# Optimization experiments

Hardware: AMD Instinct MI355X
Metric: run time of the kernel (lower is better)

Reference implementation:

```python
import jax, jax.numpy as jnp
import numpy as np

B, T, C = 8, 512, 2048          # batch streams, qlen, hidden_size
H, Z = 32, 64                   # num_heads, head_size; A = H*Z = attention_hidden_size
A = H * Z
TMX, TDX = 32, 64               # TIME_MIX_EXTRA_DIM, TIME_DECAY_EXTRA_DIM
EPS = 1e-5 * 8.0**2             # ln_x eps = 1e-5 * head_size_divisor**2


def setup_inputs() -> dict:
    key = jax.random.key(0)
    ks = jax.random.split(key, 24)
    def rn(i, shape, scale=1.0):
        return jax.random.normal(ks[i], shape, jnp.float32) * scale
    inv_c = 1.0 / np.sqrt(C)
    return {
        "hidden_states": rn(0, (B * T, C)),
        "positions": jnp.zeros((B * T,), jnp.int32),
        "input_kv_state": jnp.zeros((B, H, Z, Z), jnp.float32),
        "input_shift_state": rn(1, (B, C)),
        "time_maa_x": rn(2, (1, 1, C), 0.1),
        "time_maa_w": rn(3, (1, 1, C), 0.1),
        "time_maa_k": rn(4, (1, 1, C), 0.1),
        "time_maa_v": rn(5, (1, 1, C), 0.1),
        "time_maa_r": rn(6, (1, 1, C), 0.1),
        "time_maa_g": rn(7, (1, 1, C), 0.1),
        "time_maa_w1": rn(8, (C, TMX * 5), inv_c),
        "time_maa_w2": rn(9, (5, TMX, C), 1.0 / np.sqrt(TMX)),
        "time_decay": rn(10, (1, 1, A), 0.5),
        "time_decay_w1": rn(11, (C, TDX), inv_c),
        "time_decay_w2": rn(12, (TDX, A), 0.01),
        "time_faaaa": rn(13, (H, Z), 0.1),
        "W_r": rn(14, (C, A), inv_c),
        "W_k": rn(15, (C, A), inv_c),
        "W_v": rn(16, (C, A), inv_c),
        "W_g": rn(17, (C, A), inv_c),
        "W_o": rn(18, (A, C), inv_c),
        "ln_w": 1.0 + rn(19, (C,), 0.1),
        "ln_b": rn(20, (C,), 0.1),
    }


def _rwkv6_forward(hidden_states, positions, input_kv_state, input_shift_state,
                   time_maa_x, time_maa_w, time_maa_k, time_maa_v, time_maa_r,
                   time_maa_g, time_maa_w1, time_maa_w2, time_decay,
                   time_decay_w1, time_decay_w2, time_faaaa,
                   W_r, W_k, W_v, W_g, W_o, ln_w, ln_b):
    x = hidden_states.reshape(B, T, C)
    pos0_is_zero = positions.reshape(B, T)[:, 0] == 0
    reset = jnp.where(pos0_is_zero, -100.0, 0.0)  # [B]
    # kill shift state for fresh sequences (matches * exp(-100))
    shift = input_shift_state * jnp.exp(reset)[:, None]  # [B, C]

    # token-shift mixing (shift state broadcast over T, as in source)
    xx = shift[:, None, :] - x  # [B, T, C]
    xxx = x + xx * time_maa_x
    mix = jnp.tanh(xxx @ time_maa_w1).reshape(B, T, 5, TMX)
    mix = jnp.einsum('btfe,fec->fbtc', mix, time_maa_w2)  # [5, B, T, C]
    mw, mk, mv, mr, mg = mix

    td_in = x + xx * (time_maa_w + mw)
    kx = x + xx * (time_maa_k + mk)
    vx = x + xx * (time_maa_v + mv)
    rx = x + xx * (time_maa_r + mr)
    gx = x + xx * (time_maa_g + mg)

    r = rx @ W_r
    k = kx @ W_k
    v = vx @ W_v
    g = jax.nn.silu(gx @ W_g)  # [B, T, A]

    w = time_decay + jnp.tanh(td_in @ time_decay_w1) @ time_decay_w2
    w = -jnp.exp(w.astype(jnp.float32))  # log-decay, [B, T, A]

    # split heads -> [T, B, H, Z] for scan
    def to_tbhz(a):
        return a.reshape(B, T, H, Z).transpose(1, 0, 2, 3)
    r_s, k_s, v_s, w_s = to_tbhz(r), to_tbhz(k), to_tbhz(v), to_tbhz(w)
    # zero out carried state at t=0 for fresh sequences
    w_s = w_s.at[0].add(reset[:, None, None])

    u = time_faaaa  # [H, Z]

    def step(S, rkvw):
        # S: [B, H, K, V] (key-dim x value-dim state)
        r_t, k_t, v_t, w_t = rkvw  # each [B, H, Z]
        kv = k_t[..., :, None] * v_t[..., None, :]  # [B, H, K, V]
        o = jnp.einsum('bhk,bhkv->bhv', r_t, S + u[None, :, :, None] * kv)
        S = jnp.exp(w_t)[..., None] * S + kv
        return S, o

    S_out, o = jax.lax.scan(step, input_kv_state, (r_s, k_s, v_s, w_s))
    xo = o.transpose(1, 0, 2, 3).reshape(B * T, C)  # [B*T, C]

    # GroupNorm over heads (num_groups = H)
    xg = xo.reshape(B * T, H, Z)
    mu = xg.mean(-1, keepdims=True)
    var = xg.var(-1, keepdims=True)
    xn = ((xg - mu) * jax.lax.rsqrt(var + EPS)).reshape(B * T, C) * ln_w + ln_b

    out = (xn.reshape(B, T, C) * g) @ W_o  # [B, T, C]
    return out.reshape(B * T, C)


def reference(hidden_states, positions, input_kv_state, input_shift_state,
              time_maa_x, time_maa_w, time_maa_k, time_maa_v, time_maa_r,
              time_maa_g, time_maa_w1, time_maa_w2, time_decay,
              time_decay_w1, time_decay_w2, time_faaaa,
              W_r, W_k, W_v, W_g, W_o, ln_w, ln_b):
    return _rwkv6_forward(hidden_states, positions, input_kv_state,
                          input_shift_state, time_maa_x, time_maa_w,
                          time_maa_k, time_maa_v, time_maa_r, time_maa_g,
                          time_maa_w1, time_maa_w2, time_decay, time_decay_w1,
                          time_decay_w2, time_faaaa, W_r, W_k, W_v, W_g, W_o,
                          ln_w, ln_b)
```

## Files before the change

### kernel.cpp

```cpp
#include <hip/hip_runtime.h>
#include <cmath>

#define NB 8
#define NT 512
#define NC 2048
#define NH 32
#define NZ 64
static constexpr float GN_EPS = 1e-5f * 64.0f;

typedef _Float16 f16;
typedef __attribute__((ext_vector_type(8))) _Float16 f16x8;
typedef __attribute__((ext_vector_type(4))) _Float16 f16x4;
typedef __attribute__((ext_vector_type(4))) float f4;

static __device__ __forceinline__ void gload16(const void* gp, void* lp) {
  __builtin_amdgcn_global_load_lds(
      (const __attribute__((address_space(1))) void*)gp,
      (__attribute__((address_space(3))) void*)lp, 16, 0, 0);
}

__global__ void k_transpose_cast(const float* __restrict__ in, f16* __restrict__ out,
                                 int R, int Cc) {
  __shared__ float tile[32][33];
  int c0 = blockIdx.x * 32, r0 = blockIdx.y * 32;
  int tx = threadIdx.x, ty = threadIdx.y;
#pragma unroll
  for (int i = 0; i < 4; ++i)
    tile[ty + i * 8][tx] = in[(size_t)(r0 + ty + i * 8) * Cc + c0 + tx];
  __syncthreads();
#pragma unroll
  for (int i = 0; i < 4; ++i)
    out[(size_t)(c0 + ty + i * 8) * R + r0 + tx] = (f16)tile[tx][ty + i * 8];
}

__global__ void k_transpose_split(const float* __restrict__ in, f16* __restrict__ ohi,
                                  f16* __restrict__ olo, int R, int Cc) {
  __shared__ float tile[32][33];
  int c0 = blockIdx.x * 32, r0 = blockIdx.y * 32;
  int tx = threadIdx.x, ty = threadIdx.y;
#pragma unroll
  for (int i = 0; i < 4; ++i)
    tile[ty + i * 8][tx] = in[(size_t)(r0 + ty + i * 8) * Cc + c0 + tx];
  __syncthreads();
#pragma unroll
  for (int i = 0; i < 4; ++i) {
    float v = tile[tx][ty + i * 8];
    f16 h = (f16)v;
    size_t o = (size_t)(c0 + ty + i * 8) * R + r0 + tx;
    ohi[o] = h;
    olo[o] = (f16)(v - (float)h);
  }
}

__global__ void k_xxx(const float* __restrict__ hs, const float* __restrict__ shift_st,
                      const int* __restrict__ positions, const float* __restrict__ maa_x,
                      float* __restrict__ xxx) {
  int i = blockIdx.x * blockDim.x + threadIdx.x;
  int idx = i * 4;
  int c = idx & (NC - 1);
  int t = idx >> 11;
  int b = t >> 9;
  float er = (positions[b * NT] == 0) ? expf(-100.0f) : 1.0f;
  const float4 x = *(const float4*)(hs + idx);
  const float4 sh = *(const float4*)(shift_st + b * NC + c);
  const float4 mx = *(const float4*)(maa_x + c);
  float4 o;
  o.x = x.x + (sh.x * er - x.x) * mx.x;
  o.y = x.y + (sh.y * er - x.y) * mx.y;
  o.z = x.z + (sh.z * er - x.z) * mx.z;
  o.w = x.w + (sh.w * er - x.w) * mx.w;
  *(float4*)(xxx + idx) = o;
}

static __device__ __forceinline__ void split4(const float4 v, int base, f16x8& hi, f16x8& lo) {
  float x[4] = {v.x, v.y, v.z, v.w};
#pragma unroll
  for (int j = 0; j < 4; ++j) {
    f16 h = (f16)x[j];
    hi[base + j] = h;
    lo[base + j] = (f16)(x[j] - (float)h);
  }
}

__global__ __launch_bounds__(64) void k_mix1_split(const float* __restrict__ A,
                                                   const f16* __restrict__ Bhi,
                                                   const f16* __restrict__ Blo,
                                                   float* __restrict__ out) {
  int m0 = blockIdx.x * 16, n0 = blockIdx.y * 16;
  int lane = threadIdx.x, lr = lane & 15, kq = lane >> 4;
  f4 acc = {0.f, 0.f, 0.f, 0.f};
  const float* ap = A + (size_t)(m0 + lr) * 2048 + kq * 8;
  const f16* bh0 = Bhi + (size_t)(n0 + lr) * 2048 + kq * 8;
  const f16* bl0 = Blo + (size_t)(n0 + lr) * 2048 + kq * 8;
  for (int k0 = 0; k0 < 2048; k0 += 32) {
    f16x8 ah, al;
    split4(*(const float4*)(ap + k0), 0, ah, al);
    split4(*(const float4*)(ap + k0 + 4), 4, ah, al);
    f16x8 bh = *(const f16x8*)(bh0 + k0);
    f16x8 bl = *(const f16x8*)(bl0 + k0);
    acc = __builtin_amdgcn_mfma_f32_16x16x32_f16(ah, bh, acc, 0, 0, 0);
    acc = __builtin_amdgcn_mfma_f32_16x16x32_f16(ah, bl, acc, 0, 0, 0);
    acc = __builtin_amdgcn_mfma_f32_16x16x32_f16(al, bh, acc, 0, 0, 0);
  }
#pragma unroll
  for (int r = 0; r < 4; ++r)
    out[(size_t)(m0 + kq * 4 + r) * 160 + n0 + lr] = tanhf(acc[r]);
}

__global__ __launch_bounds__(64) void k_tmp5_split(const float* __restrict__ mixb,
    const f16* __restrict__ Bhi, const f16* __restrict__ Blo,
    const float* __restrict__ hs, const float* __restrict__ shift_st,
    const int* __restrict__ positions,
    const float* __restrict__ maa_w, const float* __restrict__ maa_k,
    const float* __restrict__ maa_v, const float* __restrict__ maa_r,
    const float* __restrict__ maa_g,
    float* __restrict__ tdin, f16* __restrict__ kx, f16* __restrict__ vx,
    f16* __restrict__ rx, f16* __restrict__ gx) {
  int m0 = blockIdx.x * 16, n0 = blockIdx.y * 16;
  int lane = threadIdx.x, lr = lane & 15, kq = lane >> 4;
  f4 acc[5];
#pragma unroll
  for (int f = 0; f < 5; ++f) acc[f] = (f4){0.f, 0.f, 0.f, 0.f};
  const float* ap = mixb + (size_t)(m0 + lr) * 160 + kq * 8;
#pragma unroll
  for (int f = 0; f < 5; ++f) {
    f16x8 ah, al;
    split4(*(const float4*)(ap + f * 32), 0, ah, al);
    split4(*(const float4*)(ap + f * 32 + 4), 4, ah, al);
    size_t bi = ((size_t)f * 2048 + n0 + lr) * 32 + kq * 8;
    f16x8 bh = *(const f16x8*)(Bhi + bi);
    f16x8 bl = *(const f16x8*)(Blo + bi);
    acc[f] = __builtin_amdgcn_mfma_f32_16x16x32_f16(ah, bh, acc[f], 0, 0, 0);
    acc[f] = __builtin_amdgcn_mfma_f32_16x16x32_f16(ah, bl, acc[f], 0, 0, 0);
    acc[f] = __builtin_amdgcn_mfma_f32_16x16x32_f16(al, bh, acc[f], 0, 0, 0);
  }
  int c = n0 + lr;
  float mw = maa_w[c], mk = maa_k[c], mv = maa_v[c], mr = maa_r[c], mg = maa_g[c];
#pragma unroll
  for (int r = 0; r < 4; ++r) {
    int t = m0 + kq * 4 + r;
    int b = t >> 9;
    float er = (positions[b * NT] == 0) ? expf(-100.0f) : 1.0f;
    float x = hs[(size_t)t * NC + c];
    float xxv = shift_st[b * NC + c] * er - x;
    size_t oi = (size_t)t * NC + c;
    tdin[oi] = x + xxv * (mw + acc[0][r]);
    kx[oi] = (f16)(x + xxv * (mk + acc[1][r]));
    vx[oi] = (f16)(x + xxv * (mv + acc[2][r]));
    rx[oi] = (f16)(x + xxv * (mr + acc[3][r]));
    gx[oi] = (f16)(x + xxv * (mg + acc[4][r]));
  }
}

__global__ __launch_bounds__(64) void k_wd1_split(const float* __restrict__ A,
                                                  const f16* __restrict__ Bhi,
                                                  const f16* __restrict__ Blo,
                                                  float* __restrict__ out) {
  int m0 = blockIdx.x * 16, n0 = blockIdx.y * 16;
  int lane = threadIdx.x, lr = lane & 15, kq = lane >> 4;
  f4 acc = {0.f, 0.f, 0.f, 0.f};
  const float* ap = A + (size_t)(m0 + lr) * 2048 + kq * 8;
  const f16* bh0 = Bhi + (size_t)(n0 + lr) * 2048 + kq * 8;
  const f16* bl0 = Blo + (size_t)(n0 + lr) * 2048 + kq * 8;
  for (int k0 = 0; k0 < 2048; k0 += 32) {
    f16x8 ah, al;
    split4(*(const float4*)(ap + k0), 0, ah, al);
    split4(*(const float4*)(ap + k0 + 4), 4, ah, al);
    f16x8 bh = *(const f16x8*)(bh0 + k0);
    f16x8 bl = *(const f16x8*)(bl0 + k0);
    acc = __builtin_amdgcn_mfma_f32_16x16x32_f16(ah, bh, acc, 0, 0, 0);
    acc = __builtin_amdgcn_mfma_f32_16x16x32_f16(ah, bl, acc, 0, 0, 0);
    acc = __builtin_amdgcn_mfma_f32_16x16x32_f16(al, bh, acc, 0, 0, 0);
  }
#pragma unroll
  for (int r = 0; r < 4; ++r)
    out[(size_t)(m0 + kq * 4 + r) * 64 + n0 + lr] = tanhf(acc[r]);
}

__global__ __launch_bounds__(64) void k_wdecay_split(const float* __restrict__ A,
                                                     const f16* __restrict__ Bhi,
                                                     const f16* __restrict__ Blo,
                                                     const float* __restrict__ time_decay,
                                                     float* __restrict__ wout) {
  int m0 = blockIdx.x * 16, n0 = blockIdx.y * 16;
  int lane = threadIdx.x, lr = lane & 15, kq = lane >> 4;
  f4 acc = {0.f, 0.f, 0.f, 0.f};
#pragma unroll
  for (int kk = 0; kk < 2; ++kk) {
    f16x8 ah, al;
    const float* ap = A + (size_t)(m0 + lr) * 64 + kk * 32 + kq * 8;
    split4(*(const float4*)ap, 0, ah, al);
    split4(*(const float4*)(ap + 4), 4, ah, al);
    size_t bi = (size_t)(n0 + lr) * 64 + kk * 32 + kq * 8;
    f16x8 bh = *(const f16x8*)(Bhi + bi);
    f16x8 bl = *(const f16x8*)(Blo + bi);
    acc = __builtin_amdgcn_mfma_f32_16x16x32_f16(ah, bh, acc, 0, 0, 0);
    acc = __builtin_amdgcn_mfma_f32_16x16x32_f16(ah, bl, acc, 0, 0, 0);
    acc = __builtin_amdgcn_mfma_f32_16x16x32_f16(al, bh, acc, 0, 0, 0);
  }
  int c = n0 + lr;
  float td = time_decay[c];
#pragma unroll
  for (int r = 0; r < 4; ++r) {
    int t = m0 + kq * 4 + r;
    wout[(size_t)t * NC + c] = -expf(td + acc[r]);
  }
}

#define GBM 128
#define GBN 128
#define GBK 64

template <int EPI>
__global__ __launch_bounds__(256) void k_gemm_big(const f16* __restrict__ A,
                                                  const f16* __restrict__ Bt,
                                                  float* __restrict__ Cf,
                                                  f16* __restrict__ Cb, int K) {
  __shared__ __align__(16) f16 As[GBM][GBK];
  __shared__ __align__(16) f16 Bs[GBN][GBK];
  int n0 = blockIdx.x * GBN, m0 = blockIdx.y * GBM;
  int tid = threadIdx.x;
  int wid = tid >> 6, lane = tid & 63;
  int wr = wid >> 1, wc = wid & 1;
  int lr = lane & 15, kq = lane >> 4;
  const f16* aL = A + (size_t)(m0 + wid * 32 + (lane >> 3)) * K + (lane & 7) * 8;
  const f16* bL = Bt + (size_t)(n0 + wid * 32 + (lane >> 3)) * K + (lane & 7) * 8;
  f4 acc[4][4];
#pragma unroll
  for (int m = 0; m < 4; ++m)
#pragma unroll
    for (int n = 0; n < 4; ++n) acc[m][n] = (f4){0.f, 0.f, 0.f, 0.f};

  int niter = K / GBK;
  for (int it = 0; it < niter; ++it) {
    int k0 = it * GBK;
    __syncthreads();
#pragma unroll
    for (int i = 0; i < 4; ++i) {
      gload16(aL + k0 + (size_t)i * 8 * K, &As[wid * 32 + i * 8][0]);
      gload16(bL + k0 + (size_t)i * 8 * K, &Bs[wid * 32 + i * 8][0]);
    }
    __syncthreads();
#pragma unroll
    for (int kk = 0; kk < 2; ++kk) {
      f16x8 af[4], bfv[4];
#pragma unroll
      for (int m = 0; m < 4; ++m)
        af[m] = *(const f16x8*)&As[wr * 64 + m * 16 + lr][kk * 32 + kq * 8];
#pragma unroll
      for (int n = 0; n < 4; ++n)
        bfv[n] = *(const f16x8*)&Bs[wc * 64 + n * 16 + lr][kk * 32 + kq * 8];
#pragma unroll
      for (int m = 0; m < 4; ++m)
#pragma unroll
        for (int n = 0; n < 4; ++n)
          acc[m][n] = __builtin_amdgcn_mfma_f32_16x16x32_f16(af[m], bfv[n], acc[m][n], 0, 0, 0);
    }
  }
#pragma unroll
  for (int m = 0; m < 4; ++m) {
    int row0 = m0 + wr * 64 + m * 16 + kq * 4;
#pragma unroll
    for (int n = 0; n < 4; ++n) {
      int col = n0 + wc * 64 + n * 16 + lr;
#pragma unroll
      for (int r = 0; r < 4; ++r) {
        float v = acc[m][n][r];
        size_t oi = (size_t)(row0 + r) * NC + col;
        if (EPI == 0) {
          Cf[oi] = v;
        } else {
          float s = v / (1.0f + expf(-v));
          Cb[oi] = (f16)s;
        }
      }
    }
  }
}

__global__ __launch_bounds__(64) void k_scanB(
    const float* rb, const float* __restrict__ kb,
    const float* __restrict__ vb, const float* __restrict__ wb,
    const float* __restrict__ kvstate, const int* __restrict__ positions,
    const float* __restrict__ faaaa, f16* __restrict__ o,
    float* rtil, float* __restrict__ Ebuf, float* __restrict__ Dbuf) {
  int blk = blockIdx.x;
  int bh = blk >> 3, c = blk & 7;
  int b = bh >> 5, h = bh & 31;
  int zz = threadIdx.x;
  __shared__ __align__(16) float shR[64];
  __shared__ __align__(16) float shE[64];
  __shared__ __align__(16) float shK[64];
  float S[64];
  if (c == 0) {
    const float* S0 = kvstate + (size_t)bh * 4096;
#pragma unroll
    for (int j = 0; j < 64; ++j) S[j] = S0[j * 64 + zz];
  } else {
#pragma unroll
    for (int j = 0; j < 64; ++j) S[j] = 0.f;
  }
  float u = faaaa[h * 64 + zz];
  float reset = (positions[b * NT] == 0) ? -100.0f : 0.0f;
  const size_t base = ((size_t)(b * NT) + c * 64) * NC + h * 64 + zz;
  float vr = rb[base], vk = kb[base], vw = wb[base], vv = vb[base];
  float Pw = 1.0f;
  for (int t = 0; t < 64; ++t) {
    float nr = 0.f, nk = 0.f, nw = 0.f, nv = 0.f;
    if (t + 1 < 64) {
      size_t idx = base + (size_t)(t + 1) * NC;
      nr = rb[idx]; nk = kb[idx]; nw = wb[idx]; nv = vb[idx];
    }
    float ww = vw;
    if (c == 0 && t == 0) ww += reset;
    float ew = expf(ww);
    shR[zz] = vr; shE[zz] = ew; shK[zz] = vk;
    float q = vr * u * vk;
    q += __shfl_xor(q, 1);  q += __shfl_xor(q, 2);  q += __shfl_xor(q, 4);
    q += __shfl_xor(q, 8);  q += __shfl_xor(q, 16); q += __shfl_xor(q, 32);
    __syncthreads();
    if (c > 0) rtil[base + (size_t)t * NC] = vr * Pw;
    Pw *= ew;
    float oacc = vv * q;
#pragma unroll
    for (int k0 = 0; k0 < 64; k0 += 4) {
      f4 r4 = *(const f4*)&shR[k0];
      f4 e4 = *(const f4*)&shE[k0];
      f4 k4 = *(const f4*)&shK[k0];
#pragma unroll
      for (int j = 0; j < 4; ++j) {
        oacc = fmaf(r4[j], S[k0 + j], oacc);
        S[k0 + j] = fmaf(e4[j], S[k0 + j], k4[j] * vv);
      }
    }
    o[base + (size_t)t * NC] = (f16)oacc;
    __syncthreads();
    vr = nr; vk = nk; vw = nw; vv = nv;
  }
  if (c < 7) {
    float* E = Ebuf + ((size_t)bh * 7 + c) * 4096;
#pragma unroll
    for (int j = 0; j < 64; ++j) E[j * 64 + zz] = S[j];
  }
  Dbuf[((size_t)bh * 8 + c) * 64 + zz] = Pw;
}

__global__ __launch_bounds__(256) void k_comb(float* __restrict__ Ebuf,
                                              const float* __restrict__ Dbuf) {
  int bh = blockIdx.x, tid = threadIdx.x;
  int k = tid >> 2, v0 = (tid & 3) * 16;
  float* base = Ebuf + (size_t)bh * 7 * 4096;
  float S[16];
#pragma unroll
  for (int j = 0; j < 16; ++j) S[j] = base[k * 64 + v0 + j];
  for (int c = 2; c <= 7; ++c) {
    float d = Dbuf[((size_t)bh * 8 + (c - 1)) * 64 + k];
    float* slot = base + (size_t)(c - 1) * 4096;
#pragma unroll
    for (int j = 0; j < 16; ++j) {
      S[j] = fmaf(d, S[j], slot[k * 64 + v0 + j]);
      slot[k * 64 + v0 + j] = S[j];
    }
  }
}

__global__ __launch_bounds__(256) void k_fix(const float* __restrict__ rtil,
                                             const float* __restrict__ Ebuf,
                                             f16* __restrict__ o) {
  int blk = blockIdx.x;
  int bh = blk / 7, cm = blk - bh * 7;
  int c = cm + 1;
  int b = bh >> 5, h = bh & 31;
  __shared__ float Rs[64][65];
  __shared__ float Ss[64][65];
  int tid = threadIdx.x;
  const float* rsrc = rtil + ((size_t)(b * NT) + c * 64) * NC + h * NZ;
  const float* ssrc = Ebuf + ((size_t)bh * 7 + cm) * 4096;
#pragma unroll
  for (int q = 0; q < 4; ++q) {
    int li = tid * 4 + q;
    int rr = li >> 4, cc = (li & 15) * 4;
    float4 x = *(const float4*)(rsrc + (size_t)rr * NC + cc);
    Rs[rr][cc] = x.x; Rs[rr][cc + 1] = x.y; Rs[rr][cc + 2] = x.z; Rs[rr][cc + 3] = x.w;
    float4 y = *(const float4*)(ssrc + rr * 64 + cc);
    Ss[rr][cc] = y.x; Ss[rr][cc + 1] = y.y; Ss[rr][cc + 2] = y.z; Ss[rr][cc + 3] = y.w;
  }
  __syncthreads();
  int t = tid >> 2, v0 = (tid & 3) * 16;
  float acc[16];
#pragma unroll
  for (int j = 0; j < 16; ++j) acc[j] = 0.f;
  for (int k = 0; k < 64; ++k) {
    float rv = Rs[t][k];
#pragma unroll
    for (int j = 0; j < 16; ++j) acc[j] = fmaf(rv, Ss[k][v0 + j], acc[j]);
  }
  f16* op = o + ((size_t)(b * NT) + c * 64 + t) * NC + h * NZ + v0;
  f16x8 o0 = *(f16x8*)op, o1 = *(f16x8*)(op + 8);
#pragma unroll
  for (int j = 0; j < 8; ++j) {
    o0[j] = (f16)((float)o0[j] + acc[j]);
    o1[j] = (f16)((float)o1[j] + acc[j + 8]);
  }
  *(f16x8*)op = o0;
  *(f16x8*)(op + 8) = o1;
}

__global__ __launch_bounds__(256) void k_gnorm(const f16* __restrict__ xo, const f16* __restrict__ g,
    const float* __restrict__ ln_w, const float* __restrict__ ln_b, f16* __restrict__ y) {
  int t = blockIdx.x;
  int tid = threadIdx.x;
  int c = tid * 8;
  f16x8 xv8 = *(const f16x8*)(xo + (size_t)t * NC + c);
  float xv[8];
#pragma unroll
  for (int j = 0; j < 8; ++j) xv[j] = (float)xv8[j];
  float s = 0.f, ss = 0.f;
#pragma unroll
  for (int j = 0; j < 8; ++j) { s += xv[j]; ss += xv[j] * xv[j]; }
  s += __shfl_xor(s, 1); ss += __shfl_xor(ss, 1);
  s += __shfl_xor(s, 2); ss += __shfl_xor(ss, 2);
  s += __shfl_xor(s, 4); ss += __shfl_xor(ss, 4);
  float mu = s * (1.0f / 64.0f);
  float var = ss * (1.0f / 64.0f) - mu * mu;
  float rstd = rsqrtf(var + GN_EPS);
  f16x8 gv = *(const f16x8*)(g + (size_t)t * NC + c);
  f16x8 ov;
#pragma unroll
  for (int j = 0; j < 8; ++j) {
    float xn = (xv[j] - mu) * rstd * ln_w[c + j] + ln_b[c + j];
    ov[j] = (f16)(xn * (float)gv[j]);
  }
  *(f16x8*)(y + (size_t)t * NC + c) = ov;
}

extern "C" void kernel_launch(void* const* d_in, const int* in_sizes, int n_in,
                              void* d_out, int out_size, void* d_ws, size_t ws_size,
                              hipStream_t stream) {
  const float* hs = (const float*)d_in[0];
  const int* positions = (const int*)d_in[1];
  const float* kvstate = (const float*)d_in[2];
  const float* shift_st = (const float*)d_in[3];
  const float* maa_x = (const float*)d_in[4];
  const float* maa_w = (const float*)d_in[5];
  const float* maa_k = (const float*)d_in[6];
  const float* maa_v = (const float*)d_in[7];
  const float* maa_r = (const float*)d_in[8];
  const float* maa_g = (const float*)d_in[9];
  const float* maa_w1 = (const float*)d_in[10];
  const float* maa_w2 = (const float*)d_in[11];
  const float* time_decay = (const float*)d_in[12];
  const float* decay_w1 = (const float*)d_in[13];
  const float* decay_w2 = (const float*)d_in[14];
  const float* faaaa = (const float*)d_in[15];
  const float* W_r = (const float*)d_in[16];
  const float* W_k = (const float*)d_in[17];
  const float* W_v = (const float*)d_in[18];
  const float* W_g = (const float*)d_in[19];
  const float* W_o = (const float*)d_in[20];
  const float* ln_w = (const float*)d_in[21];
  const float* ln_b = (const float*)d_in[22];

  char* ws = (char*)d_ws;
  size_t off = 0;
  auto alloc = [&](size_t n) {
    char* p = ws + off;
    off += (n + 255) & ~(size_t)255;
    return p;
  };
  f16* w1t_hi = (f16*)alloc(160ull * 2048 * 2);
  f16* w1t_lo = (f16*)alloc(160ull * 2048 * 2);
  f16* w2t_hi = (f16*)alloc(5ull * 2048 * 32 * 2);
  f16* w2t_lo = (f16*)alloc(5ull * 2048 * 32 * 2);
  f16* dw1t_hi = (f16*)alloc(64ull * 2048 * 2);
  f16* dw1t_lo = (f16*)alloc(64ull * 2048 * 2);
  f16* dw2t_hi = (f16*)alloc(2048ull * 64 * 2);
  f16* dw2t_lo = (f16*)alloc(2048ull * 64 * 2);
  float* mixb = (float*)alloc(4096ull * 160 * 4);
  float* wd1 = (float*)alloc(4096ull * 64 * 4);
  char* R_A = alloc(4096ull * 2048 * 4);
  char* R_B = alloc(4096ull * 2048 * 4);
  char* R_C = alloc(4096ull * 2048 * 4);
  char* R_D = alloc(4096ull * 2048 * 4);
  char* R_E = alloc(4096ull * 2048 * 2);
  char* F12 = alloc(4096ull * 2048 * 4);
  char* F3 = alloc(4096ull * 2048 * 2);
  char* F4 = alloc(4096ull * 2048 * 2);

  float* xxx = (float*)R_A;
  float* tdin = (float*)R_A;
  float* wbuf = (float*)R_A;
  float* rbuf = (float*)R_B;
  float* kbuf = (float*)R_C;
  float* vbuf = (float*)R_D;
  f16* wstage = (f16*)R_E;
  f16* obuf = (f16*)R_E;
  f16* kx = (f16*)F12;
  f16* vx = (f16*)(F12 + 4096ull * 2048 * 2);
  float* Ebuf = (float*)F12;
  float* Dbuf = (float*)(F12 + 29360128);
  f16* rx = (f16*)F3;
  f16* gbuf = (f16*)F3;
  f16* gx = (f16*)F4;
  f16* wt_o = (f16*)F4;

  dim3 tb(32, 8);
  k_transpose_split<<<dim3(5, 64), tb, 0, stream>>>(maa_w1, w1t_hi, w1t_lo, 2048, 160);
  for (int f = 0; f < 5; ++f)
    k_transpose_split<<<dim3(64, 1), tb, 0, stream>>>(maa_w2 + (size_t)f * 32 * 2048,
        w2t_hi + (size_t)f * 2048 * 32, w2t_lo + (size_t)f * 2048 * 32, 32, 2048);
  k_transpose_split<<<dim3(2, 64), tb, 0, stream>>>(decay_w1, dw1t_hi, dw1t_lo, 2048, 64);
  k_transpose_split<<<dim3(64, 2), tb, 0, stream>>>(decay_w2, dw2t_hi, dw2t_lo, 64, 2048);

  k_xxx<<<8192, 256, 0, stream>>>(hs, shift_st, positions, maa_x, xxx);
  k_mix1_split<<<dim3(256, 10), 64, 0, stream>>>(xxx, w1t_hi, w1t_lo, mixb);
  k_tmp5_split<<<dim3(256, 128), 64, 0, stream>>>(mixb, w2t_hi, w2t_lo, hs, shift_st,
      positions, maa_w, maa_k, maa_v, maa_r, maa_g, tdin, kx, vx, rx, gx);
  k_wd1_split<<<dim3(256, 4), 64, 0, stream>>>(tdin, dw1t_hi, dw1t_lo, wd1);
  k_wdecay_split<<<dim3(256, 128), 64, 0, stream>>>(wd1, dw2t_hi, dw2t_lo, time_decay, wbuf);

  dim3 gg(2048 / GBN, 4096 / GBM);
  k_transpose_cast<<<dim3(64, 64), tb, 0, stream>>>(W_r, wstage, 2048, 2048);
  k_gemm_big<0><<<gg, 256, 0, stream>>>(rx, wstage, rbuf, nullptr, 2048);
  k_transpose_cast<<<dim3(64, 64), tb, 0, stream>>>(W_k, wstage, 2048, 2048);
  k_gemm_big<0><<<gg, 256, 0, stream>>>(kx, wstage, kbuf, nullptr, 2048);
  k_transpose_cast<<<dim3(64, 64), tb, 0, stream>>>(W_v, wstage, 2048, 2048);
  k_gemm_big<0><<<gg, 256, 0, stream>>>(vx, wstage, vbuf, nullptr, 2048);
  k_transpose_cast<<<dim3(64, 64), tb, 0, stream>>>(W_g, wstage, 2048, 2048);
  k_gemm_big<2><<<gg, 256, 0, stream>>>(gx, wstage, nullptr, gbuf, 2048);
  k_transpose_cast<<<dim3(64, 64), tb, 0, stream>>>(W_o, wt_o, 2048, 2048);

  k_scanB<<<2048, 64, 0, stream>>>(rbuf, kbuf, vbuf, wbuf, kvstate, positions, faaaa,
                                   obuf, rbuf, Ebuf, Dbuf);
  k_comb<<<256, 256, 0, stream>>>(Ebuf, Dbuf);
  k_fix<<<1792, 256, 0, stream>>>(rbuf, Ebuf, obuf);

  k_gnorm<<<4096, 256, 0, stream>>>(obuf, gbuf, ln_w, ln_b, obuf);
  k_gemm_big<0><<<gg, 256, 0, stream>>>(obuf, wt_o, (float*)d_out, nullptr, 2048);
}
```

Measured before the change: 693.1 us.

## Double-buffer GEMM LDS with swizzle, widen skinny GEMM tiles, double-buffer scan

The main GEMM now double-buffers its LDS tiles and prefetches the next K slice while computing the current one. It also XOR-swizzles the LDS layout to avoid bank conflicts. The skinny mix1 and wd1 GEMMs now compute several 16-column output tiles per block, so each converted A fragment is reused and the A re-reads and hi/lo splitting across blocks go away, at the cost of fewer blocks. The scan kernel double-buffers its shared r/e/k arrays to drop one barrier per step, and prefetches inputs two steps ahead.

```diff
diff --git a/kernel.cpp b/kernel.cpp
--- a/kernel.cpp
+++ b/kernel.cpp
@@ -86,25 +86,32 @@
                                                    const f16* __restrict__ Bhi,
                                                    const f16* __restrict__ Blo,
                                                    float* __restrict__ out) {
-  int m0 = blockIdx.x * 16, n0 = blockIdx.y * 16;
+  int m0 = blockIdx.x * 16;
+  int half = blockIdx.y;
   int lane = threadIdx.x, lr = lane & 15, kq = lane >> 4;
-  f4 acc = {0.f, 0.f, 0.f, 0.f};
+  f4 acc[5];
+#pragma unroll
+  for (int f = 0; f < 5; ++f) acc[f] = (f4){0.f, 0.f, 0.f, 0.f};
   const float* ap = A + (size_t)(m0 + lr) * 2048 + kq * 8;
-  const f16* bh0 = Bhi + (size_t)(n0 + lr) * 2048 + kq * 8;
-  const f16* bl0 = Blo + (size_t)(n0 + lr) * 2048 + kq * 8;
   for (int k0 = 0; k0 < 2048; k0 += 32) {
     f16x8 ah, al;
     split4(*(const float4*)(ap + k0), 0, ah, al);
     split4(*(const float4*)(ap + k0 + 4), 4, ah, al);
-    f16x8 bh = *(const f16x8*)(bh0 + k0);
-    f16x8 bl = *(const f16x8*)(bl0 + k0);
-    acc = __builtin_amdgcn_mfma_f32_16x16x32_f16(ah, bh, acc, 0, 0, 0);
-    acc = __builtin_amdgcn_mfma_f32_16x16x32_f16(ah, bl, acc, 0, 0, 0);
-    acc = __builtin_amdgcn_mfma_f32_16x16x32_f16(al, bh, acc, 0, 0, 0);
-  }
-#pragma unroll
-  for (int r = 0; r < 4; ++r)
-    out[(size_t)(m0 + kq * 4 + r) * 160 + n0 + lr] = tanhf(acc[r]);
+#pragma unroll
+    for (int f = 0; f < 5; ++f) {
+      size_t bi = (size_t)((half * 5 + f) * 16 + lr) * 2048 + k0 + kq * 8;
+      f16x8 bh = *(const f16x8*)(Bhi + bi);
+      f16x8 bl = *(const f16x8*)(Blo + bi);
+      acc[f] = __builtin_amdgcn_mfma_f32_16x16x32_f16(ah, bh, acc[f], 0, 0, 0);
+      acc[f] = __builtin_amdgcn_mfma_f32_16x16x32_f16(ah, bl, acc[f], 0, 0, 0);
+      acc[f] = __builtin_amdgcn_mfma_f32_16x16x32_f16(al, bh, acc[f], 0, 0, 0);
+    }
+  }
+#pragma unroll
+  for (int f = 0; f < 5; ++f)
+#pragma unroll
+    for (int r = 0; r < 4; ++r)
+      out[(size_t)(m0 + kq * 4 + r) * 160 + (half * 5 + f) * 16 + lr] = tanhf(acc[f][r]);
 }
 
 __global__ __launch_bounds__(64) void k_tmp5_split(const float* __restrict__ mixb,
@@ -156,25 +163,31 @@
                                                   const f16* __restrict__ Bhi,
                                                   const f16* __restrict__ Blo,
                                                   float* __restrict__ out) {
-  int m0 = blockIdx.x * 16, n0 = blockIdx.y * 16;
+  int m0 = blockIdx.x * 16;
   int lane = threadIdx.x, lr = lane & 15, kq = lane >> 4;
-  f4 acc = {0.f, 0.f, 0.f, 0.f};
+  f4 acc[4];
+#pragma unroll
+  for (int f = 0; f < 4; ++f) acc[f] = (f4){0.f, 0.f, 0.f, 0.f};
   const float* ap = A + (size_t)(m0 + lr) * 2048 + kq * 8;
-  const f16* bh0 = Bhi + (size_t)(n0 + lr) * 2048 + kq * 8;
-  const f16* bl0 = Blo + (size_t)(n0 + lr) * 2048 + kq * 8;
   for (int k0 = 0; k0 < 2048; k0 += 32) {
     f16x8 ah, al;
     split4(*(const float4*)(ap + k0), 0, ah, al);
     split4(*(const float4*)(ap + k0 + 4), 4, ah, al);
-    f16x8 bh = *(const f16x8*)(bh0 + k0);
-    f16x8 bl = *(const f16x8*)(bl0 + k0);
-    acc = __builtin_amdgcn_mfma_f32_16x16x32_f16(ah, bh, acc, 0, 0, 0);
-    acc = __builtin_amdgcn_mfma_f32_16x16x32_f16(ah, bl, acc, 0, 0, 0);
-    acc = __builtin_amdgcn_mfma_f32_16x16x32_f16(al, bh, acc, 0, 0, 0);
-  }
-#pragma unroll
-  for (int r = 0; r < 4; ++r)
-    out[(size_t)(m0 + kq * 4 + r) * 64 + n0 + lr] = tanhf(acc[r]);
+#pragma unroll
+    for (int f = 0; f < 4; ++f) {
+      size_t bi = (size_t)(f * 16 + lr) * 2048 + k0 + kq * 8;
+      f16x8 bh = *(const f16x8*)(Bhi + bi);
+      f16x8 bl = *(const f16x8*)(Blo + bi);
+      acc[f] = __builtin_amdgcn_mfma_f32_16x16x32_f16(ah, bh, acc[f], 0, 0, 0);
+      acc[f] = __builtin_amdgcn_mfma_f32_16x16x32_f16(ah, bl, acc[f], 0, 0, 0);
+      acc[f] = __builtin_amdgcn_mfma_f32_16x16x32_f16(al, bh, acc[f], 0, 0, 0);
+    }
+  }
+#pragma unroll
+  for (int f = 0; f < 4; ++f)
+#pragma unroll
+    for (int r = 0; r < 4; ++r)
+      out[(size_t)(m0 + kq * 4 + r) * 64 + f * 16 + lr] = tanhf(acc[f][r]);
 }
 
 __global__ __launch_bounds__(64) void k_wdecay_split(const float* __restrict__ A,
@@ -216,46 +229,58 @@
                                                   const f16* __restrict__ Bt,
                                                   float* __restrict__ Cf,
                                                   f16* __restrict__ Cb, int K) {
-  __shared__ __align__(16) f16 As[GBM][GBK];
-  __shared__ __align__(16) f16 Bs[GBN][GBK];
+  __shared__ __align__(16) f16 As[2][GBM][GBK];
+  __shared__ __align__(16) f16 Bs[2][GBN][GBK];
   int n0 = blockIdx.x * GBN, m0 = blockIdx.y * GBM;
   int tid = threadIdx.x;
   int wid = tid >> 6, lane = tid & 63;
   int wr = wid >> 1, wc = wid & 1;
   int lr = lane & 15, kq = lane >> 4;
-  const f16* aL = A + (size_t)(m0 + wid * 32 + (lane >> 3)) * K + (lane & 7) * 8;
-  const f16* bL = Bt + (size_t)(n0 + wid * 32 + (lane >> 3)) * K + (lane & 7) * 8;
+  int sw = lr & 7;
+  int gunit = (lane & 7) ^ (lane >> 3);
+  const f16* aL = A + (size_t)(m0 + wid * 32 + (lane >> 3)) * K + gunit * 8;
+  const f16* bL = Bt + (size_t)(n0 + wid * 32 + (lane >> 3)) * K + gunit * 8;
   f4 acc[4][4];
 #pragma unroll
   for (int m = 0; m < 4; ++m)
 #pragma unroll
     for (int n = 0; n < 4; ++n) acc[m][n] = (f4){0.f, 0.f, 0.f, 0.f};
 
+#pragma unroll
+  for (int i = 0; i < 4; ++i) {
+    gload16(aL + (size_t)i * 8 * K, &As[0][wid * 32 + i * 8][0]);
+    gload16(bL + (size_t)i * 8 * K, &Bs[0][wid * 32 + i * 8][0]);
+  }
+  __syncthreads();
   int niter = K / GBK;
+  int cur = 0;
   for (int it = 0; it < niter; ++it) {
-    int k0 = it * GBK;
-    __syncthreads();
-#pragma unroll
-    for (int i = 0; i < 4; ++i) {
-      gload16(aL + k0 + (size_t)i * 8 * K, &As[wid * 32 + i * 8][0]);
-      gload16(bL + k0 + (size_t)i * 8 * K, &Bs[wid * 32 + i * 8][0]);
-    }
-    __syncthreads();
+    if (it + 1 < niter) {
+      int k0 = (it + 1) * GBK;
+#pragma unroll
+      for (int i = 0; i < 4; ++i) {
+        gload16(aL + k0 + (size_t)i * 8 * K, &As[cur ^ 1][wid * 32 + i * 8][0]);
+        gload16(bL + k0 + (size_t)i * 8 * K, &Bs[cur ^ 1][wid * 32 + i * 8][0]);
+      }
+    }
 #pragma unroll
     for (int kk = 0; kk < 2; ++kk) {
       f16x8 af[4], bfv[4];
+      int un = ((kk * 4 + kq) ^ sw) * 8;
 #pragma unroll
       for (int m = 0; m < 4; ++m)
-        af[m] = *(const f16x8*)&As[wr * 64 + m * 16 + lr][kk * 32 + kq * 8];
+        af[m] = *(const f16x8*)&As[cur][wr * 64 + m * 16 + lr][un];
 #pragma unroll
       for (int n = 0; n < 4; ++n)
-        bfv[n] = *(const f16x8*)&Bs[wc * 64 + n * 16 + lr][kk * 32 + kq * 8];
+        bfv[n] = *(const f16x8*)&Bs[cur][wc * 64 + n * 16 + lr][un];
 #pragma unroll
       for (int m = 0; m < 4; ++m)
 #pragma unroll
         for (int n = 0; n < 4; ++n)
           acc[m][n] = __builtin_amdgcn_mfma_f32_16x16x32_f16(af[m], bfv[n], acc[m][n], 0, 0, 0);
     }
+    __syncthreads();
+    cur ^= 1;
   }
 #pragma unroll
   for (int m = 0; m < 4; ++m) {
@@ -288,9 +313,9 @@
   int bh = blk >> 3, c = blk & 7;
   int b = bh >> 5, h = bh & 31;
   int zz = threadIdx.x;
-  __shared__ __align__(16) float shR[64];
-  __shared__ __align__(16) float shE[64];
-  __shared__ __align__(16) float shK[64];
+  __shared__ __align__(16) float shR[2][64];
+  __shared__ __align__(16) float shE[2][64];
+  __shared__ __align__(16) float shK[2][64];
   float S[64];
   if (c == 0) {
     const float* S0 = kvstate + (size_t)bh * 4096;
@@ -303,30 +328,33 @@
   float u = faaaa[h * 64 + zz];
   float reset = (positions[b * NT] == 0) ? -100.0f : 0.0f;
   const size_t base = ((size_t)(b * NT) + c * 64) * NC + h * 64 + zz;
-  float vr = rb[base], vk = kb[base], vw = wb[base], vv = vb[base];
+  float r0v = rb[base], k0v = kb[base], w0v = wb[base], v0v = vb[base];
+  float r1v = rb[base + NC], k1v = kb[base + NC], w1v = wb[base + NC], v1v = vb[base + NC];
   float Pw = 1.0f;
   for (int t = 0; t < 64; ++t) {
-    float nr = 0.f, nk = 0.f, nw = 0.f, nv = 0.f;
-    if (t + 1 < 64) {
-      size_t idx = base + (size_t)(t + 1) * NC;
-      nr = rb[idx]; nk = kb[idx]; nw = wb[idx]; nv = vb[idx];
-    }
-    float ww = vw;
+    float r2v = 0.f, k2v = 0.f, w2v = 0.f, v2v = 0.f;
+    if (t + 2 < 64) {
+      size_t idx = base + (size_t)(t + 2) * NC;
+      r2v = rb[idx]; k2v = kb[idx]; w2v = wb[idx]; v2v = vb[idx];
+    }
+    int p = t & 1;
+    float ww = w0v;
     if (c == 0 && t == 0) ww += reset;
     float ew = expf(ww);
-    shR[zz] = vr; shE[zz] = ew; shK[zz] = vk;
-    float q = vr * u * vk;
+    shR[p][zz] = r0v; shE[p][zz] = ew; shK[p][zz] = k0v;
+    float q = r0v * u * k0v;
     q += __shfl_xor(q, 1);  q += __shfl_xor(q, 2);  q += __shfl_xor(q, 4);
     q += __shfl_xor(q, 8);  q += __shfl_xor(q, 16); q += __shfl_xor(q, 32);
     __syncthreads();
-    if (c > 0) rtil[base + (size_t)t * NC] = vr * Pw;
+    if (c > 0) rtil[base + (size_t)t * NC] = r0v * Pw;
     Pw *= ew;
+    float vv = v0v;
     float oacc = vv * q;
 #pragma unroll
     for (int k0 = 0; k0 < 64; k0 += 4) {
-      f4 r4 = *(const f4*)&shR[k0];
-      f4 e4 = *(const f4*)&shE[k0];
-      f4 k4 = *(const f4*)&shK[k0];
+      f4 r4 = *(const f4*)&shR[p][k0];
+      f4 e4 = *(const f4*)&shE[p][k0];
+      f4 k4 = *(const f4*)&shK[p][k0];
 #pragma unroll
       for (int j = 0; j < 4; ++j) {
         oacc = fmaf(r4[j], S[k0 + j], oacc);
@@ -334,8 +362,8 @@
       }
     }
     o[base + (size_t)t * NC] = (f16)oacc;
-    __syncthreads();
-    vr = nr; vk = nk; vw = nw; vv = nv;
+    r0v = r1v; k0v = k1v; w0v = w1v; v0v = v1v;
+    r1v = r2v; k1v = k2v; w1v = w2v; v1v = v2v;
   }
   if (c < 7) {
     float* E = Ebuf + ((size_t)bh * 7 + c) * 4096;
@@ -513,10 +541,10 @@
   k_transpose_split<<<dim3(64, 2), tb, 0, stream>>>(decay_w2, dw2t_hi, dw2t_lo, 64, 2048);
 
   k_xxx<<<8192, 256, 0, stream>>>(hs, shift_st, positions, maa_x, xxx);
-  k_mix1_split<<<dim3(256, 10), 64, 0, stream>>>(xxx, w1t_hi, w1t_lo, mixb);
+  k_mix1_split<<<dim3(256, 2), 64, 0, stream>>>(xxx, w1t_hi, w1t_lo, mixb);
   k_tmp5_split<<<dim3(256, 128), 64, 0, stream>>>(mixb, w2t_hi, w2t_lo, hs, shift_st,
       positions, maa_w, maa_k, maa_v, maa_r, maa_g, tdin, kx, vx, rx, gx);
-  k_wd1_split<<<dim3(256, 4), 64, 0, stream>>>(tdin, dw1t_hi, dw1t_lo, wd1);
+  k_wd1_split<<<256, 64, 0, stream>>>(tdin, dw1t_hi, dw1t_lo, wd1);
   k_wdecay_split<<<dim3(256, 128), 64, 0, stream>>>(wd1, dw2t_hi, dw2t_lo, time_decay, wbuf);
 
   dim3 gg(2048 / GBN, 4096 / GBM);
```

After: 781.7 us. 12.8% more time.

## Double-buffer GEMM LDS tiles, XOR-swizzle LDS layout, and remap workgroups

Applied to the files above, without the earlier changes.

The big GEMM kernel now keeps two LDS buffers and prefetches the next K tile while MFMAs run on the current one, which removes one barrier per iteration. LDS rows are XOR-swizzled on the 16-byte unit index to reduce bank conflicts on fragment reads. Workgroup IDs are remapped so that groups running together share operand tiles in cache. This doubles LDS use to 64KB per block, which may lower occupancy.

```diff
diff --git a/kernel.cpp b/kernel.cpp
--- a/kernel.cpp
+++ b/kernel.cpp
@@ -216,46 +216,62 @@
                                                   const f16* __restrict__ Bt,
                                                   float* __restrict__ Cf,
                                                   f16* __restrict__ Cb, int K) {
-  __shared__ __align__(16) f16 As[GBM][GBK];
-  __shared__ __align__(16) f16 Bs[GBN][GBK];
-  int n0 = blockIdx.x * GBN, m0 = blockIdx.y * GBM;
+  __shared__ __align__(16) f16 As[2][GBM][GBK];
+  __shared__ __align__(16) f16 Bs[2][GBN][GBK];
+  int nwg = gridDim.x * gridDim.y;
+  int wg = blockIdx.y * gridDim.x + blockIdx.x;
+  int swz = (wg & 7) * (nwg >> 3) + (wg >> 3);
+  int n0 = (swz % gridDim.x) * GBN;
+  int m0 = (swz / gridDim.x) * GBM;
   int tid = threadIdx.x;
   int wid = tid >> 6, lane = tid & 63;
   int wr = wid >> 1, wc = wid & 1;
   int lr = lane & 15, kq = lane >> 4;
-  const f16* aL = A + (size_t)(m0 + wid * 32 + (lane >> 3)) * K + (lane & 7) * 8;
-  const f16* bL = Bt + (size_t)(n0 + wid * 32 + (lane >> 3)) * K + (lane & 7) * 8;
+  int sw = lr & 7;
+  int gunit = (lane & 7) ^ (lane >> 3);
+  const f16* aL = A + (size_t)(m0 + wid * 32 + (lane >> 3)) * K + gunit * 8;
+  const f16* bL = Bt + (size_t)(n0 + wid * 32 + (lane >> 3)) * K + gunit * 8;
   f4 acc[4][4];
 #pragma unroll
   for (int m = 0; m < 4; ++m)
 #pragma unroll
     for (int n = 0; n < 4; ++n) acc[m][n] = (f4){0.f, 0.f, 0.f, 0.f};
 
+#pragma unroll
+  for (int i = 0; i < 4; ++i) {
+    gload16(aL + (size_t)i * 8 * K, &As[0][wid * 32 + i * 8][0]);
+    gload16(bL + (size_t)i * 8 * K, &Bs[0][wid * 32 + i * 8][0]);
+  }
+  __syncthreads();
   int niter = K / GBK;
+  int cur = 0;
   for (int it = 0; it < niter; ++it) {
-    int k0 = it * GBK;
-    __syncthreads();
-#pragma unroll
-    for (int i = 0; i < 4; ++i) {
-      gload16(aL + k0 + (size_t)i * 8 * K, &As[wid * 32 + i * 8][0]);
-      gload16(bL + k0 + (size_t)i * 8 * K, &Bs[wid * 32 + i * 8][0]);
+    if (it + 1 < niter) {
+      int k0 = (it + 1) * GBK;
+#pragma unroll
+      for (int i = 0; i < 4; ++i) {
+        gload16(aL + k0 + (size_t)i * 8 * K, &As[cur ^ 1][wid * 32 + i * 8][0]);
+        gload16(bL + k0 + (size_t)i * 8 * K, &Bs[cur ^ 1][wid * 32 + i * 8][0]);
+      }
     }
-    __syncthreads();
 #pragma unroll
     for (int kk = 0; kk < 2; ++kk) {
       f16x8 af[4], bfv[4];
+      int un = ((kk * 4 + kq) ^ sw) * 8;
 #pragma unroll
       for (int m = 0; m < 4; ++m)
-        af[m] = *(const f16x8*)&As[wr * 64 + m * 16 + lr][kk * 32 + kq * 8];
+        af[m] = *(const f16x8*)&As[cur][wr * 64 + m * 16 + lr][un];
 #pragma unroll
       for (int n = 0; n < 4; ++n)
-        bfv[n] = *(const f16x8*)&Bs[wc * 64 + n * 16 + lr][kk * 32 + kq * 8];
+        bfv[n] = *(const f16x8*)&Bs[cur][wc * 64 + n * 16 + lr][un];
 #pragma unroll
       for (int m = 0; m < 4; ++m)
 #pragma unroll
         for (int n = 0; n < 4; ++n)
           acc[m][n] = __builtin_amdgcn_mfma_f32_16x16x32_f16(af[m], bfv[n], acc[m][n], 0, 0, 0);
     }
+    __syncthreads();
+    cur ^= 1;
   }
 #pragma unroll
   for (int m = 0; m < 4; ++m) {
```

Measured after the change: 654.6 us. -5.6%, faster.
